# Kernel optimization log

Hardware: AMD Instinct MI355X
Metric: run time of the kernel (lower is better)

## Reference

```python
import jax, jax.numpy as jnp
import numpy as np


def setup_inputs() -> dict:
    key = jax.random.key(0)
    k1, k2, k3 = jax.random.split(key, 3)
    B, S, E = 4, 8192, 1024
    x = jax.random.normal(k1, (B, S, E), dtype=jnp.float32)
    # torch nn.Linear weights have shape [out_features, in_features]
    W1 = jax.random.normal(k2, (3 * E, E), dtype=jnp.float32) * (1.0 / np.sqrt(E))
    W2 = jax.random.normal(k3, (E, E), dtype=jnp.float32) * (1.0 / np.sqrt(E))
    return {"x": x, "W1": W1, "W2": W2, "heads": 16}


def reference(x, W1, W2, heads):
    B, S, E = x.shape
    h = heads
    e = E // h
    # qkv projection: [B,S,3E] -> 'b s (n h e) -> n b h s e'
    qkv = (x @ W1.T).reshape(B, S, 3, h, e)
    qkv = jnp.transpose(qkv, (2, 0, 3, 1, 4))  # [3,B,h,S,e]
    q, k, v = qkv[0], qkv[1], qkv[2]
    # score: [B,h,e,e], softmax over last dim (c)
    score = jax.nn.softmax(jnp.einsum('bhnk,bhnc->bhkc', k / 4, v), axis=-1)
    # einsum 'bhnk,bhkc->bhnk': elementwise over k, sum over c
    attn = jax.nn.softmax(jnp.einsum('bhnk,bhkc->bhnk', q / 4, score), axis=-1)
    # 'b h s e -> b s (h e)' then linear_2
    out = jnp.transpose(attn, (0, 2, 1, 3)).reshape(B, S, E) @ W2.T
    return out
```

## Files before the change

### kernel.cpp

```cpp
#include <hip/hip_runtime.h>
#include <hip/hip_bf16.h>
#include <stdint.h>

static constexpr int MTOT = 32768;
static constexpr int KD   = 1024;
static constexpr int ND   = 1024;

static constexpr int BM = 256, BN = 256, BK = 64;
static constexpr int NT = KD / BK;
static constexpr int BUF_BYTES = 65536;
static constexpr int BOFF = 32768;
static constexpr int HALF = 16384;

typedef __bf16 bf16x8 __attribute__((ext_vector_type(8)));
typedef float  f32x4  __attribute__((ext_vector_type(4)));

__device__ __forceinline__ unsigned short f2bf_rne(float f) {
  union { float f; uint32_t u; } c; c.f = f;
  uint32_t u = c.u;
  return (unsigned short)((u + 0x7fffu + ((u >> 16) & 1u)) >> 16);
}

__global__ void cast_f32_to_bf16(const float* __restrict__ src,
                                 unsigned short* __restrict__ dst, int n4) {
  int idx = blockIdx.x * blockDim.x + threadIdx.x;
  int stride = gridDim.x * blockDim.x;
  for (int i = idx; i < n4; i += stride) {
    float4 v = reinterpret_cast<const float4*>(src)[i];
    ushort4 o;
    o.x = f2bf_rne(v.x); o.y = f2bf_rne(v.y);
    o.z = f2bf_rne(v.z); o.w = f2bf_rne(v.w);
    reinterpret_cast<ushort4*>(dst)[i] = o;
  }
}

__device__ __forceinline__ void gload_lds16(const void* g, void* lds) {
  __builtin_amdgcn_global_load_lds(
      (const __attribute__((address_space(1))) unsigned int*)g,
      (__attribute__((address_space(3))) unsigned int*)lds, 16, 0, 0);
}

template <int SOFTMAX>
__global__ __launch_bounds__(512, 2)
void gemm8(const unsigned short* __restrict__ A,
           const unsigned short* __restrict__ Bm,
           void* __restrict__ Cout) {
  extern __shared__ __align__(16) char ldsc[];

  const int tid  = threadIdx.x;
  const int lane = tid & 63;
  const int wid  = tid >> 6;
  const int wm = wid >> 2, wn = wid & 3;
  const int fr = lane & 15, fq = lane >> 4;

  const int bid0 = blockIdx.x;
  const int bid  = ((bid0 & 7) << 6) | (bid0 >> 3);
  const int brow = (bid >> 2) * BM;
  const int bcol = (bid & 3) * BN;

  const int srow  = tid >> 3;
  const int sslot = (tid & 7) ^ (srow & 7);
  const unsigned short* gA = A  + (size_t)(brow + srow) * KD + sslot * 8;
  const unsigned short* gB = Bm + (size_t)(bcol + srow) * KD + sslot * 8;

  f32x4  acc[8][4] = {};
  bf16x8 a0[4][2], a1[4][2], bA[2][2], bB[2][2];

  auto STAGE = [&](const unsigned short* g, int h, int kt, int b, int opOff) {
    const unsigned short* gu = g + (size_t)(h * 128) * KD + kt * BK;
    char* du = ldsc + b * BUF_BYTES + opOff + h * HALF + (wid << 10);
    gload_lds16(gu, du);
    gload_lds16(gu + (size_t)64 * KD, du + 8192);
  };

  auto rdA = [&](int b, bf16x8 (*dst)[2], int mBase) {
    const char* base = ldsc + b * BUF_BYTES + wm * HALF;
    #pragma unroll
    for (int mm = 0; mm < 4; ++mm) {
      const int r = (mBase + mm) * 16 + fr;
      #pragma unroll
      for (int ks = 0; ks < 2; ++ks)
        dst[mm][ks] = *(const bf16x8*)(base + (r << 7) +
                        ((ks * 64 + fq * 16) ^ ((r & 7) << 4)));
    }
  };
  auto rdB = [&](int b, int nBase, bf16x8 (*dst)[2]) {
    const char* base = ldsc + b * BUF_BYTES + BOFF + (wn >> 1) * HALF;
    #pragma unroll
    for (int nn = 0; nn < 2; ++nn) {
      const int r = (wn & 1) * 64 + (nBase + nn) * 16 + fr;
      #pragma unroll
      for (int ks = 0; ks < 2; ++ks)
        dst[nn][ks] = *(const bf16x8*)(base + (r << 7) +
                       ((ks * 64 + fq * 16) ^ ((r & 7) << 4)));
    }
  };
  auto MFMA16 = [&](int mBase, int nBase, bf16x8 (*af)[2], bf16x8 (*bf)[2]) {
    __builtin_amdgcn_s_setprio(1);
    #pragma unroll
    for (int ks = 0; ks < 2; ++ks)
      #pragma unroll
      for (int mm = 0; mm < 4; ++mm)
        #pragma unroll
        for (int nn = 0; nn < 2; ++nn)
          acc[mBase + mm][nBase + nn] = __builtin_amdgcn_mfma_f32_16x16x32_bf16(
              af[mm][ks], bf[nn][ks], acc[mBase + mm][nBase + nn], 0, 0, 0);
    __builtin_amdgcn_s_setprio(0);
  };

  auto tileStep = [&](int T, int cur, int nxt) {
    const int tp1 = (T + 1 < NT) ? T + 1 : NT - 1;
    const int tp2 = (T + 2 < NT) ? T + 2 : NT - 1;

    rdA(cur, a0, 0);
    rdA(cur, a1, 4);
    STAGE(gB, 0, tp1, nxt, BOFF);
    STAGE(gB, 1, tp1, nxt, BOFF);
    MFMA16(0, 0, a0, bA);

    MFMA16(4, 0, a1, bA);
    __builtin_amdgcn_s_barrier();

    rdB(cur, 2, bB);
    STAGE(gA, 0, tp2, cur, 0);
    MFMA16(4, 2, a1, bB);

    STAGE(gA, 1, tp2, cur, 0);
    asm volatile("s_waitcnt vmcnt(4)" ::: "memory");
    __builtin_amdgcn_s_barrier();
    rdB(nxt, 0, bA);
    MFMA16(0, 2, a0, bB);
    __builtin_amdgcn_s_barrier();
  };

  STAGE(gA, 0, 0, 0, 0);    STAGE(gA, 1, 0, 0, 0);
  STAGE(gB, 0, 0, 0, BOFF); STAGE(gB, 1, 0, 0, BOFF);
  STAGE(gA, 0, 1, 1, 0);    STAGE(gA, 1, 1, 1, 0);
  asm volatile("s_waitcnt vmcnt(4)" ::: "memory");
  __builtin_amdgcn_s_barrier();
  rdB(0, 0, bA);

  for (int T = 0; T < NT; T += 2) {
    tileStep(T,     0, 1);
    tileStep(T + 1, 1, 0);
  }

  if constexpr (SOFTMAX) {
    unsigned short* attn = reinterpret_cast<unsigned short*>(Cout);
    constexpr float CEXP = 0.25f * 1.44269504088896340736f;
    #pragma unroll
    for (int m = 0; m < 8; ++m) {
      const int row = brow + wm * 128 + m * 16 + fq * 4;
      #pragma unroll
      for (int j = 0; j < 4; ++j) {
        float v0 = acc[m][0][j], v1 = acc[m][1][j];
        float v2 = acc[m][2][j], v3 = acc[m][3][j];
        float mx = fmaxf(fmaxf(v0, v1), fmaxf(v2, v3));
        #pragma unroll
        for (int s = 1; s < 16; s <<= 1) mx = fmaxf(mx, __shfl_xor(mx, s, 64));
        float p0 = exp2f((v0 - mx) * CEXP);
        float p1 = exp2f((v1 - mx) * CEXP);
        float p2 = exp2f((v2 - mx) * CEXP);
        float p3 = exp2f((v3 - mx) * CEXP);
        float sm = p0 + p1 + p2 + p3;
        #pragma unroll
        for (int s = 1; s < 16; s <<= 1) sm += __shfl_xor(sm, s, 64);
        const float inv = 1.0f / sm;
        unsigned short* dst =
            attn + (size_t)(row + j) * ND + (bcol + wn * 64 + fr);
        dst[0]  = f2bf_rne(p0 * inv);
        dst[16] = f2bf_rne(p1 * inv);
        dst[32] = f2bf_rne(p2 * inv);
        dst[48] = f2bf_rne(p3 * inv);
      }
    }
  } else {
    float* Cf = reinterpret_cast<float*>(Cout);
    #pragma unroll
    for (int m = 0; m < 8; ++m) {
      const int row = brow + wm * 128 + m * 16 + fq * 4;
      #pragma unroll
      for (int n = 0; n < 4; ++n) {
        const int col = bcol + wn * 64 + n * 16 + fr;
        #pragma unroll
        for (int j = 0; j < 4; ++j)
          Cf[(size_t)(row + j) * ND + col] = acc[m][n][j];
      }
    }
  }
}

extern "C" void kernel_launch(void* const* d_in, const int* in_sizes, int n_in,
                              void* d_out, int out_size, void* d_ws, size_t ws_size,
                              hipStream_t stream) {
  const float* x  = (const float*)d_in[0];
  const float* W1 = (const float*)d_in[1];
  const float* W2 = (const float*)d_in[2];
  float* out = (float*)d_out;

  char* ws = (char*)d_ws;
  unsigned short* xb   = (unsigned short*)(ws);
  unsigned short* w1b  = (unsigned short*)(ws + (size_t)67108864);
  unsigned short* w2b  = (unsigned short*)(ws + (size_t)69206016);
  unsigned short* attn = (unsigned short*)(ws + (size_t)71303168);

  hipFuncSetAttribute(reinterpret_cast<const void*>(gemm8<1>),
                      hipFuncAttributeMaxDynamicSharedMemorySize, 131072);
  hipFuncSetAttribute(reinterpret_cast<const void*>(gemm8<0>),
                      hipFuncAttributeMaxDynamicSharedMemorySize, 131072);

  cast_f32_to_bf16<<<2048, 256, 0, stream>>>(x,  xb,  MTOT * KD / 4);
  cast_f32_to_bf16<<<512,  256, 0, stream>>>(W1, w1b, KD * KD / 4);
  cast_f32_to_bf16<<<512,  256, 0, stream>>>(W2, w2b, KD * KD / 4);

  const int nblk = (MTOT / BM) * (ND / BN);
  gemm8<1><<<nblk, 512, 131072, stream>>>(xb, w1b, (void*)attn);
  gemm8<0><<<nblk, 512, 131072, stream>>>(attn, w2b, (void*)out);
}
```

Baseline: 189.3 us.

## Merge cast kernels, reorder tile staging, and stage fp32 epilogue through LDS

Replaces the three cast launches with one kernel that walks x, W1 and W2 in a single grid-stride loop, removing two launch gaps. Moves one B-tile stage and the first MFMA group ahead of the second A-fragment read to change the overlap of loads and math. In the fp32 GEMM epilogue, each wave writes its accumulators into LDS and reads them back so it can issue contiguous 16-byte row stores instead of scattered 4-byte stores. The LDS round trip adds waits, and the per-wave 16KB regions reuse the pipeline buffers after the main loop with no block barrier.

```diff
diff --git a/kernel.cpp b/kernel.cpp
--- a/kernel.cpp
+++ b/kernel.cpp
@@ -21,16 +21,27 @@
   return (unsigned short)((u + 0x7fffu + ((u >> 16) & 1u)) >> 16);
 }
 
-__global__ void cast_f32_to_bf16(const float* __restrict__ src,
-                                 unsigned short* __restrict__ dst, int n4) {
+__global__ void cast_all(const float* __restrict__ x,
+                         const float* __restrict__ W1,
+                         const float* __restrict__ W2,
+                         unsigned short* __restrict__ xb,
+                         unsigned short* __restrict__ w1b,
+                         unsigned short* __restrict__ w2b) {
+  constexpr int n4x = MTOT * KD / 4;
+  constexpr int n4w = KD * KD / 4;
+  constexpr int total = n4x + 2 * n4w;
   int idx = blockIdx.x * blockDim.x + threadIdx.x;
   int stride = gridDim.x * blockDim.x;
-  for (int i = idx; i < n4; i += stride) {
-    float4 v = reinterpret_cast<const float4*>(src)[i];
+  for (int i = idx; i < total; i += stride) {
+    const float* s; unsigned short* d; int j;
+    if (i < n4x)            { s = x;  d = xb;  j = i; }
+    else if (i < n4x + n4w) { s = W1; d = w1b; j = i - n4x; }
+    else                    { s = W2; d = w2b; j = i - n4x - n4w; }
+    float4 v = reinterpret_cast<const float4*>(s)[j];
     ushort4 o;
     o.x = f2bf_rne(v.x); o.y = f2bf_rne(v.y);
     o.z = f2bf_rne(v.z); o.w = f2bf_rne(v.w);
-    reinterpret_cast<ushort4*>(dst)[i] = o;
+    reinterpret_cast<ushort4*>(d)[j] = o;
   }
 }
 
@@ -113,11 +124,11 @@
     const int tp2 = (T + 2 < NT) ? T + 2 : NT - 1;
 
     rdA(cur, a0, 0);
+    STAGE(gB, 0, tp1, nxt, BOFF);
+    MFMA16(0, 0, a0, bA);
+
     rdA(cur, a1, 4);
-    STAGE(gB, 0, tp1, nxt, BOFF);
     STAGE(gB, 1, tp1, nxt, BOFF);
-    MFMA16(0, 0, a0, bA);
-
     MFMA16(4, 0, a1, bA);
     __builtin_amdgcn_s_barrier();
 
@@ -176,16 +187,29 @@
     }
   } else {
     float* Cf = reinterpret_cast<float*>(Cout);
-    #pragma unroll
-    for (int m = 0; m < 8; ++m) {
-      const int row = brow + wm * 128 + m * 16 + fq * 4;
-      #pragma unroll
-      for (int n = 0; n < 4; ++n) {
-        const int col = bcol + wn * 64 + n * 16 + fr;
-        #pragma unroll
-        for (int j = 0; j < 4; ++j)
-          Cf[(size_t)(row + j) * ND + col] = acc[m][n][j];
+    char* wlds = ldsc + wid * 16384;
+    #pragma unroll
+    for (int h = 0; h < 2; ++h) {
+      asm volatile("" ::: "memory");
+      #pragma unroll
+      for (int mm = 0; mm < 4; ++mm)
+        #pragma unroll
+        for (int n = 0; n < 4; ++n)
+          #pragma unroll
+          for (int j = 0; j < 4; ++j)
+            *(float*)(wlds + (((mm * 16 + fq * 4 + j) << 6) + n * 16 + fr) * 4)
+                = acc[4 * h + mm][n][j];
+      asm volatile("s_waitcnt lgkmcnt(0)" ::: "memory");
+      const int rbase = brow + wm * 128 + h * 64;
+      #pragma unroll
+      for (int i = 0; i < 16; ++i) {
+        const int idx16 = i * 64 + lane;
+        const int rl = idx16 >> 4;
+        const int c4 = (idx16 & 15) << 2;
+        f32x4 v = *(const f32x4*)(wlds + (size_t)idx16 * 16);
+        *(f32x4*)(&Cf[(size_t)(rbase + rl) * ND + (bcol + wn * 64 + c4)]) = v;
       }
+      asm volatile("s_waitcnt lgkmcnt(0)" ::: "memory");
     }
   }
 }
@@ -209,9 +233,7 @@
   hipFuncSetAttribute(reinterpret_cast<const void*>(gemm8<0>),
                       hipFuncAttributeMaxDynamicSharedMemorySize, 131072);
 
-  cast_f32_to_bf16<<<2048, 256, 0, stream>>>(x,  xb,  MTOT * KD / 4);
-  cast_f32_to_bf16<<<512,  256, 0, stream>>>(W1, w1b, KD * KD / 4);
-  cast_f32_to_bf16<<<512,  256, 0, stream>>>(W2, w2b, KD * KD / 4);
+  cast_all<<<2048, 256, 0, stream>>>(x, W1, W2, xb, w1b, w2b);
 
   const int nblk = (MTOT / BM) * (ND / BN);
   gemm8<1><<<nblk, 512, 131072, stream>>>(xb, w1b, (void*)attn);
```

Result: faster. 185.4 us (-2.1%).
